# Kernel optimization log

Measured on AMD Instinct MI355X. Metric: run time of the kernel, lower is better.

## Reference

```python
import jax, jax.numpy as jnp
import numpy as np

N, E = 50000, 800000
IN, H1, H2, HEADS, EMB = 128, 32, 32, 4, 128
NEG_SLOPE = 0.2  # DGL GATConv default leaky_relu slope


def setup_inputs() -> dict:
    key = jax.random.key(0)
    ks = jax.random.split(key, 14)
    s = 0.05
    return {
        "x": jax.random.normal(ks[0], (N, IN), jnp.float32),
        "src": jax.random.randint(ks[1], (E,), 0, N, jnp.int32),
        "dst": jax.random.randint(ks[2], (E,), 0, N, jnp.int32),
        "W1": jax.random.normal(ks[3], (IN, HEADS * H1), jnp.float32) * s,
        "al1": jax.random.normal(ks[4], (HEADS, H1), jnp.float32) * s,
        "ar1": jax.random.normal(ks[5], (HEADS, H1), jnp.float32) * s,
        "b1": jnp.zeros((HEADS * H1,), jnp.float32),
        "W2": jax.random.normal(ks[6], (HEADS * H1, HEADS * H2), jnp.float32) * s,
        "al2": jax.random.normal(ks[7], (HEADS, H2), jnp.float32) * s,
        "ar2": jax.random.normal(ks[8], (HEADS, H2), jnp.float32) * s,
        "b2": jnp.zeros((HEADS * H2,), jnp.float32),
        "Wp": jax.random.normal(ks[9], (HEADS * H2, EMB), jnp.float32) * s,
        "bp": jnp.zeros((EMB,), jnp.float32),
    }


def gat_layer(x, W, al, ar, b, src, dst, heads, d_out):
    n = x.shape[0]
    feat = (x @ W).reshape(n, heads, d_out)            # [N,H,D]
    el = (feat * al).sum(-1)                           # [N,H]
    er = (feat * ar).sum(-1)                           # [N,H]
    e = jax.nn.leaky_relu(el[src] + er[dst], NEG_SLOPE)  # [E,H]
    # edge softmax over destination segments
    m = jax.ops.segment_max(e, dst, num_segments=n)    # [N,H] (-inf for empty)
    ex = jnp.exp(e - m[dst])                           # [E,H]
    z = jax.ops.segment_sum(ex, dst, num_segments=n)   # [N,H]
    alpha = ex / z[dst]                                # [E,H]
    msg = alpha[:, :, None] * feat[src]                # [E,H,D]
    out = jax.ops.segment_sum(msg, dst, num_segments=n)  # [N,H,D]
    return out + b.reshape(1, heads, d_out)


def reference(x, src, dst, W1, al1, ar1, b1, W2, al2, ar2, b2, Wp, bp):
    h = gat_layer(x, W1, al1, ar1, b1, src, dst, HEADS, H1).reshape(N, -1)
    h = gat_layer(h, W2, al2, ar2, b2, src, dst, HEADS, H2).reshape(N, -1)
    out = h @ Wp + bp
    return (h, out)
```

## Files before the change

### kernel.cpp

```cpp
#include <hip/hip_runtime.h>
#include <hip/hip_bf16.h>

#define N_NODES 50000
#define HEADS 4
#define DHEAD 32
#define F 128
#define NEG_SLOPE 0.2f
#define MAXD 64

typedef unsigned int uint;
typedef unsigned short ushort;
typedef __attribute__((ext_vector_type(8))) short bf16x8;
typedef __attribute__((ext_vector_type(4))) float f32x4;

__device__ __forceinline__ float bf2f(ushort u) {
    union { uint i; float f; } c; c.i = ((uint)u) << 16; return c.f;
}
__device__ __forceinline__ ushort f2bf(float f) {
    union { float f; uint i; } c; c.f = f;
    uint u = c.i + 0x7FFF + ((c.i >> 16) & 1);
    return (ushort)(u >> 16);
}
__device__ __forceinline__ float sel4(int h, float a, float b, float c, float d) {
    return (h & 2) ? ((h & 1) ? d : c) : ((h & 1) ? b : a);
}

__global__ void rank_hist_wtrans_kernel(
    const int* __restrict__ dst, int* __restrict__ counts, int* __restrict__ rank,
    const float* __restrict__ W1, const float* __restrict__ W2,
    const float* __restrict__ Wp,
    const float* __restrict__ al1, const float* __restrict__ ar1,
    const float* __restrict__ al2, const float* __restrict__ ar2,
    ushort* __restrict__ WT, int E, int EB) {
    if (blockIdx.x < (uint)EB) {
        int i = blockIdx.x * 256 + threadIdx.x;
        if (i < E) rank[i] = atomicAdd(&counts[dst[i]], 1);
        return;
    }
    int bid = blockIdx.x - EB;
    if (bid < 3) {
        const float* W = (bid == 0) ? W1 : (bid == 1) ? W2 : Wp;
        ushort* T = WT + (size_t)bid * 128 * 128;
        for (int i = threadIdx.x; i < 128 * 128; i += 256) {
            int r = i >> 7, c = i & 127;
            T[c * 128 + r] = f2bf(W[i]);
        }
    } else {
        const float* W   = (bid == 3) ? W1 : W2;
        const float* a_l = (bid == 3) ? al1 : al2;
        const float* a_r = (bid == 3) ? ar1 : ar2;
        ushort* T = WT + 3 * 128 * 128 + (bid - 3) * 16 * 128;
        for (int i = threadIdx.x; i < 16 * 128; i += 256) {
            int c = i >> 7, k = i & 127;
            float v = 0.f;
            if (c < 8) {
                int h = c & 3;
                const float* a  = (c < 4) ? (a_l + h * 32) : (a_r + h * 32);
                const float* wr = W + k * 128 + h * 32;
#pragma unroll
                for (int d = 0; d < 32; d++) v += wr[d] * a[d];
            }
            T[i] = f2bf(v);
        }
    }
}

__global__ __launch_bounds__(256) void scanA_kernel(const int* __restrict__ counts,
                                                    int* __restrict__ local_sc,
                                                    int* __restrict__ partials, int N) {
    int i = blockIdx.x * 256 + threadIdx.x;
    int v = (i < N) ? counts[i] : 0;
    int lane = threadIdx.x & 63;
    int w = threadIdx.x >> 6;
    int x = v;
#pragma unroll
    for (int off = 1; off < 64; off <<= 1) {
        int t = __shfl_up(x, off);
        if (lane >= off) x += t;
    }
    __shared__ int wsum[4];
    if (lane == 63) wsum[w] = x;
    __syncthreads();
    int wpre = 0;
#pragma unroll
    for (int k = 0; k < 4; k++)
        if (k < w) wpre += wsum[k];
    if (i < N) local_sc[i] = x - v + wpre;
    if (threadIdx.x == 255) partials[blockIdx.x] = wpre + x;
}

__global__ void scanB_kernel(int* __restrict__ partials, int NP) {
    int tid = threadIdx.x;
    int v = (tid < NP) ? partials[tid] : 0;
    int lane = tid & 63;
    int w = tid >> 6;
    int x = v;
#pragma unroll
    for (int off = 1; off < 64; off <<= 1) {
        int t = __shfl_up(x, off);
        if (lane >= off) x += t;
    }
    __shared__ int wsum[4];
    if (lane == 63) wsum[w] = x;
    __syncthreads();
    int wpre = 0;
#pragma unroll
    for (int k = 0; k < 4; k++)
        if (k < w) wpre += wsum[k];
    if (tid < NP) partials[tid] = x - v + wpre;
}

__global__ __launch_bounds__(256) void scanC_kernel(int* __restrict__ offs,
                                                    const int* __restrict__ partials,
                                                    int N, int E) {
    int i = blockIdx.x * 256 + threadIdx.x;
    if (i < N) offs[i] += partials[blockIdx.x];
    if (i == 0) offs[N] = E;
}

__global__ void posfix_kernel(const int* __restrict__ dst, const int* __restrict__ offs,
                              int* __restrict__ rank, int E) {
    int i = blockIdx.x * 256 + threadIdx.x;
    if (i < E) rank[i] += offs[dst[i]];
}

#define SCH 2048
__global__ __launch_bounds__(256) void scatter_ranged_kernel(
    const int* __restrict__ src, const int* __restrict__ pos,
    int* __restrict__ csr_src, int E) {
    int range = blockIdx.x & 7;
    int chunk = blockIdx.x >> 3;
    int base = chunk * SCH + threadIdx.x;
    int lo = (int)(((long long)range * E) >> 3);
    int hi = (int)(((long long)(range + 1) * E) >> 3);
#pragma unroll
    for (int k = 0; k < SCH / 256; k++) {
        int i = base + k * 256;
        if (i < E) {
            int p = pos[i];
            if (p >= lo && p < hi) csr_src[p] = src[i];
        }
    }
}

template <bool A_FP32, bool OUT_BF16, bool BIAS, bool ELER>
__global__ __launch_bounds__(256) void mfma_gemm_kernel(
    const void* __restrict__ Av, const ushort* __restrict__ BT,
    const float* __restrict__ bias, const ushort* __restrict__ ALR,
    void* __restrict__ Cv, float* __restrict__ el, float* __restrict__ er, int M) {
    int wid = threadIdx.x >> 6;
    int lane = threadIdx.x & 63;
    int row0 = blockIdx.x * 64 + wid * 16;
    int rsub = lane & 15;
    int kg = lane >> 4;
    int row = row0 + rsub;
    int rowc = (row < M) ? row : (M - 1);

    bf16x8 af[4];
    if (A_FP32) {
        const float* A = (const float*)Av;
        const float* ap = A + (size_t)rowc * 128 + kg * 8;
#pragma unroll
        for (int ks = 0; ks < 4; ks++) {
            float4 lo = *(const float4*)(ap + ks * 32);
            float4 hi = *(const float4*)(ap + ks * 32 + 4);
            bf16x8 v;
            v[0] = (short)f2bf(lo.x); v[1] = (short)f2bf(lo.y);
            v[2] = (short)f2bf(lo.z); v[3] = (short)f2bf(lo.w);
            v[4] = (short)f2bf(hi.x); v[5] = (short)f2bf(hi.y);
            v[6] = (short)f2bf(hi.z); v[7] = (short)f2bf(hi.w);
            af[ks] = v;
        }
    } else {
        const ushort* A = (const ushort*)Av;
        const ushort* ap = A + (size_t)rowc * 128 + kg * 8;
#pragma unroll
        for (int ks = 0; ks < 4; ks++) af[ks] = *(const bf16x8*)(ap + ks * 32);
    }

    f32x4 acc[8];
#pragma unroll
    for (int ct = 0; ct < 8; ct++) acc[ct] = (f32x4){0.f, 0.f, 0.f, 0.f};

    const ushort* bp = BT + (size_t)rsub * 128 + kg * 8;
#pragma unroll
    for (int ks = 0; ks < 4; ks++) {
#pragma unroll
        for (int ct = 0; ct < 8; ct++) {
            bf16x8 bf = *(const bf16x8*)(bp + (size_t)ct * 16 * 128 + ks * 32);
            acc[ct] = __builtin_amdgcn_mfma_f32_16x16x32_bf16(af[ks], bf, acc[ct], 0, 0, 0);
        }
    }

    f32x4 acce = (f32x4){0.f, 0.f, 0.f, 0.f};
    if (ELER) {
        const ushort* ep = ALR + rsub * 128 + kg * 8;
#pragma unroll
        for (int ks = 0; ks < 4; ks++) {
            bf16x8 eb = *(const bf16x8*)(ep + ks * 32);
            acce = __builtin_amdgcn_mfma_f32_16x16x32_bf16(af[ks], eb, acce, 0, 0, 0);
        }
    }

    if (row0 >= M) return;

#pragma unroll
    for (int ct = 0; ct < 8; ct++) {
        int col = ct * 16 + rsub;
        float bv = BIAS ? bias[col] : 0.f;
#pragma unroll
        for (int r = 0; r < 4; r++) {
            int gr = row0 + kg * 4 + r;
            if (gr < M) {
                float v = acc[ct][r] + bv;
                if (OUT_BF16) ((ushort*)Cv)[(size_t)gr * 128 + col] = f2bf(v);
                else          ((float*)Cv)[(size_t)gr * 128 + col] = v;
            }
        }
    }

    if (ELER && rsub < 8) {
#pragma unroll
        for (int r = 0; r < 4; r++) {
            int gr = row0 + kg * 4 + r;
            if (gr < M) {
                if (rsub < 4) el[(size_t)gr * 4 + rsub] = acce[r];
                else          er[(size_t)gr * 4 + (rsub - 4)] = acce[r];
            }
        }
    }
}

template <bool F32OUT>
__global__ __launch_bounds__(256) void aggregate_kernel(
    const ushort* __restrict__ featb, const float* __restrict__ el,
    const float* __restrict__ er, const float* __restrict__ bias,
    const int* __restrict__ offsets, const int* __restrict__ csr_src,
    void* __restrict__ outv, int N) {
    __shared__ int   s_sv[16][MAXD + 1];
    __shared__ float s_lg[16][MAXD + 1][4];
    int tid = threadIdx.x;
    int gl = tid & 15;
    int g  = tid >> 4;
    int lane = tid & 63;
    int n = blockIdx.x * 16 + g;
    if (n >= N) return;
    int start = offsets[n], end = offsets[n + 1];
    int deg = end - start;
    bool fast = (deg <= MAXD);

    float4 erv = *(const float4*)(er + (size_t)n * 4);
    float er_h[4] = {erv.x, erv.y, erv.z, erv.w};

    float m[4], s[4];
#pragma unroll
    for (int h = 0; h < 4; h++) { m[h] = -1e30f; s[h] = 0.f; }

    for (int e = start + gl; e < end; e += 16) {
        int sv = csr_src[e];
        float4 ev = *(const float4*)(el + (size_t)sv * 4);
        float elh[4] = {ev.x, ev.y, ev.z, ev.w};
        int idx = e - start;
        if (fast) s_sv[g][idx] = sv;
#pragma unroll
        for (int h = 0; h < 4; h++) {
            float v = elh[h] + er_h[h];
            v = (v >= 0.f) ? v : NEG_SLOPE * v;
            if (fast) s_lg[g][idx][h] = v;
            float mn = fmaxf(m[h], v);
            s[h] = s[h] * __expf(m[h] - mn) + __expf(v - mn);
            m[h] = mn;
        }
    }
#pragma unroll
    for (int off = 1; off < 16; off <<= 1) {
#pragma unroll
        for (int h = 0; h < 4; h++) {
            float mo = __shfl_xor(m[h], off);
            float so = __shfl_xor(s[h], off);
            float mn = fmaxf(m[h], mo);
            s[h] = s[h] * __expf(m[h] - mn) + so * __expf(mo - mn);
            m[h] = mn;
        }
    }

    int h0 = gl >> 2;
    int c0 = gl * 8;
    float acc[8] = {};

    if (fast) {
        float rz[4];
#pragma unroll
        for (int h = 0; h < 4; h++) rz[h] = (deg > 0) ? 1.0f / s[h] : 0.f;
        for (int e = gl; e < deg; e += 16) {
#pragma unroll
            for (int h = 0; h < 4; h++)
                s_lg[g][e][h] = __expf(s_lg[g][e][h] - m[h]) * rz[h];
        }
        for (int e0 = 0; e0 < deg; e0 += 8) {
            int nb = deg - e0; if (nb > 8) nb = 8;
            float av[8]; int svv[8];
#pragma unroll
            for (int jj = 0; jj < 8; jj++) {
                int idx = (jj < nb) ? (e0 + jj) : e0;
                svv[jj] = s_sv[g][idx];
                av[jj] = (jj < nb) ? s_lg[g][idx][h0] : 0.f;
            }
#pragma unroll
            for (int jj = 0; jj < 8; jj++) {
                uint4 f0 = *(const uint4*)(featb + (size_t)svv[jj] * 128 + c0);
                acc[0] = fmaf(av[jj], bf2f(f0.x & 0xFFFF), acc[0]);
                acc[1] = fmaf(av[jj], bf2f(f0.x >> 16),    acc[1]);
                acc[2] = fmaf(av[jj], bf2f(f0.y & 0xFFFF), acc[2]);
                acc[3] = fmaf(av[jj], bf2f(f0.y >> 16),    acc[3]);
                acc[4] = fmaf(av[jj], bf2f(f0.z & 0xFFFF), acc[4]);
                acc[5] = fmaf(av[jj], bf2f(f0.z >> 16),    acc[5]);
                acc[6] = fmaf(av[jj], bf2f(f0.w & 0xFFFF), acc[6]);
                acc[7] = fmaf(av[jj], bf2f(f0.w >> 16),    acc[7]);
            }
        }
    } else {
        float mh  = sel4(h0, m[0], m[1], m[2], m[3]);
        float sh  = sel4(h0, s[0], s[1], s[2], s[3]);
        float rzh = (deg > 0) ? 1.0f / sh : 0.f;
        int j = gl & 3;
        float erh = sel4(h0, er_h[0], er_h[1], er_h[2], er_h[3]);
        int bidx = lane & 60;
        for (int e = start; e < end; e += 4) {
            int rem = end - e;
            int ej = e + ((j < rem) ? j : 0);
            int svj = csr_src[ej];
            float v = el[(size_t)svj * 4 + h0] + erh;
            v = (v >= 0.f) ? v : NEG_SLOPE * v;
            float a = __expf(v - mh) * rzh;
            if (j >= rem) a = 0.f;
#pragma unroll
            for (int jj = 0; jj < 4; jj++) {
                float ajj = __shfl(a, bidx | jj);
                int svjj  = __shfl(svj, bidx | jj);
                uint4 f0 = *(const uint4*)(featb + (size_t)svjj * 128 + c0);
                acc[0] = fmaf(ajj, bf2f(f0.x & 0xFFFF), acc[0]);
                acc[1] = fmaf(ajj, bf2f(f0.x >> 16),    acc[1]);
                acc[2] = fmaf(ajj, bf2f(f0.y & 0xFFFF), acc[2]);
                acc[3] = fmaf(ajj, bf2f(f0.y >> 16),    acc[3]);
                acc[4] = fmaf(ajj, bf2f(f0.z & 0xFFFF), acc[4]);
                acc[5] = fmaf(ajj, bf2f(f0.z >> 16),    acc[5]);
                acc[6] = fmaf(ajj, bf2f(f0.w & 0xFFFF), acc[6]);
                acc[7] = fmaf(ajj, bf2f(f0.w >> 16),    acc[7]);
            }
        }
    }

    float4 b0 = *(const float4*)(bias + c0);
    float4 b1 = *(const float4*)(bias + c0 + 4);
    float o[8];
    o[0] = acc[0] + b0.x; o[1] = acc[1] + b0.y; o[2] = acc[2] + b0.z; o[3] = acc[3] + b0.w;
    o[4] = acc[4] + b1.x; o[5] = acc[5] + b1.y; o[6] = acc[6] + b1.z; o[7] = acc[7] + b1.w;
    if (F32OUT) {
        float* outf = (float*)outv;
        float4 w0, w1;
        w0.x = o[0]; w0.y = o[1]; w0.z = o[2]; w0.w = o[3];
        w1.x = o[4]; w1.y = o[5]; w1.z = o[6]; w1.w = o[7];
        *(float4*)(outf + (size_t)n * 128 + c0) = w0;
        *(float4*)(outf + (size_t)n * 128 + c0 + 4) = w1;
    } else {
        ushort* outb = (ushort*)outv;
        uint4 p;
        p.x = (uint)f2bf(o[0]) | ((uint)f2bf(o[1]) << 16);
        p.y = (uint)f2bf(o[2]) | ((uint)f2bf(o[3]) << 16);
        p.z = (uint)f2bf(o[4]) | ((uint)f2bf(o[5]) << 16);
        p.w = (uint)f2bf(o[6]) | ((uint)f2bf(o[7]) << 16);
        *(uint4*)(outb + (size_t)n * 128 + c0) = p;
    }
}

extern "C" void kernel_launch(void* const* d_in, const int* in_sizes, int n_in,
                              void* d_out, int out_size, void* d_ws, size_t ws_size,
                              hipStream_t stream) {
    const float* x   = (const float*)d_in[0];
    const int*   src = (const int*)d_in[1];
    const int*   dst = (const int*)d_in[2];
    const float* W1  = (const float*)d_in[3];
    const float* al1 = (const float*)d_in[4];
    const float* ar1 = (const float*)d_in[5];
    const float* b1  = (const float*)d_in[6];
    const float* W2  = (const float*)d_in[7];
    const float* al2 = (const float*)d_in[8];
    const float* ar2 = (const float*)d_in[9];
    const float* b2  = (const float*)d_in[10];
    const float* Wp  = (const float*)d_in[11];
    const float* bp  = (const float*)d_in[12];

    const int N = in_sizes[0] / F;
    const int E = in_sizes[1];

    float* h_out = (float*)d_out;
    float* p_out = h_out + (size_t)N * F;

    const int NB = (N + 255) / 256;
    const int EB = (E + 255) / 256;

    char* w = (char*)d_ws;
    ushort* featb   = (ushort*)w;
    ushort* h1b     = featb + (size_t)N * F;
    float* el       = (float*)(h1b + (size_t)N * F);
    float* er       = el + (size_t)N * 4;
    int*   offs     = (int*)(er + (size_t)N * 4);
    int*   counts   = offs + (N + 1);
    int*   rank     = counts + N;
    int*   csrsrc   = rank + E;
    int*   partials = csrsrc + E;
    ushort* WT      = (ushort*)(partials + 256);

    ushort* WT1  = WT;
    ushort* WT2  = WT + 128 * 128;
    ushort* WTp  = WT + 2 * 128 * 128;
    ushort* ALR1 = WT + 3 * 128 * 128;
    ushort* ALR2 = ALR1 + 16 * 128;

    hipMemsetAsync(counts, 0, (size_t)N * 4, stream);
    rank_hist_wtrans_kernel<<<EB + 5, 256, 0, stream>>>(
        dst, counts, rank, W1, W2, Wp, al1, ar1, al2, ar2, WT, E, EB);
    scanA_kernel<<<NB, 256, 0, stream>>>(counts, offs, partials, N);
    scanB_kernel<<<1, 256, 0, stream>>>(partials, NB);
    scanC_kernel<<<NB, 256, 0, stream>>>(offs, partials, N, E);
    posfix_kernel<<<EB, 256, 0, stream>>>(dst, offs, rank, E);
    scatter_ranged_kernel<<<8 * ((E + SCH - 1) / SCH), 256, 0, stream>>>(src, rank, csrsrc, E);

    int ggrid = (N + 63) / 64;
    int agrid = (N + 15) / 16;

    mfma_gemm_kernel<true, true, false, true><<<ggrid, 256, 0, stream>>>(
        x, WT1, nullptr, ALR1, featb, el, er, N);
    aggregate_kernel<false><<<agrid, 256, 0, stream>>>(
        featb, el, er, b1, offs, csrsrc, h1b, N);

    mfma_gemm_kernel<false, true, false, true><<<ggrid, 256, 0, stream>>>(
        h1b, WT2, nullptr, ALR2, featb, el, er, N);
    aggregate_kernel<true><<<agrid, 256, 0, stream>>>(
        featb, el, er, b2, offs, csrsrc, h_out, N);

    mfma_gemm_kernel<true, false, true, false><<<ggrid, 256, 0, stream>>>(
        h_out, WTp, bp, nullptr, p_out, nullptr, nullptr, N);
}
```

Baseline: 239.4 us.

## Build CSR with range-partitioned atomic cursors instead of per-edge rank arrays

Measured after the change: 256.0 us. 6.9% more time.

```diff
diff --git a/kernel.cpp b/kernel.cpp
--- a/kernel.cpp
+++ b/kernel.cpp
@@ -7,6 +7,7 @@
 #define F 128
 #define NEG_SLOPE 0.2f
 #define MAXD 64
+#define SCH 2048
 
 typedef unsigned int uint;
 typedef unsigned short ushort;
@@ -25,19 +26,30 @@
     return (h & 2) ? ((h & 1) ? d : c) : ((h & 1) ? b : a);
 }
 
-__global__ void rank_hist_wtrans_kernel(
-    const int* __restrict__ dst, int* __restrict__ counts, int* __restrict__ rank,
+__global__ void hist_ranged_wtrans_kernel(
+    const int* __restrict__ dst, int* __restrict__ counts,
     const float* __restrict__ W1, const float* __restrict__ W2,
     const float* __restrict__ Wp,
     const float* __restrict__ al1, const float* __restrict__ ar1,
     const float* __restrict__ al2, const float* __restrict__ ar2,
-    ushort* __restrict__ WT, int E, int EB) {
-    if (blockIdx.x < (uint)EB) {
-        int i = blockIdx.x * 256 + threadIdx.x;
-        if (i < E) rank[i] = atomicAdd(&counts[dst[i]], 1);
+    ushort* __restrict__ WT, int E, int N, int EC) {
+    if (blockIdx.x < (uint)(8 * EC)) {
+        int range = blockIdx.x & 7;
+        int chunk = blockIdx.x >> 3;
+        int base = chunk * SCH + threadIdx.x;
+        int nlo = (int)(((long long)range * N) >> 3);
+        int nhi = (int)(((long long)(range + 1) * N) >> 3);
+#pragma unroll
+        for (int k = 0; k < SCH / 256; k++) {
+            int i = base + k * 256;
+            if (i < E) {
+                int d = dst[i];
+                if (d >= nlo && d < nhi) atomicAdd(&counts[d], 1);
+            }
+        }
         return;
     }
-    int bid = blockIdx.x - EB;
+    int bid = blockIdx.x - 8 * EC;
     if (bid < 3) {
         const float* W = (bid == 0) ? W1 : (bid == 1) ? W2 : Wp;
         ushort* T = WT + (size_t)bid * 128 * 128;
@@ -111,34 +123,35 @@
 }
 
 __global__ __launch_bounds__(256) void scanC_kernel(int* __restrict__ offs,
+                                                    int* __restrict__ cursor,
                                                     const int* __restrict__ partials,
                                                     int N, int E) {
     int i = blockIdx.x * 256 + threadIdx.x;
-    if (i < N) offs[i] += partials[blockIdx.x];
+    if (i < N) {
+        int o = offs[i] + partials[blockIdx.x];
+        offs[i] = o;
+        cursor[i] = o;
+    }
     if (i == 0) offs[N] = E;
 }
 
-__global__ void posfix_kernel(const int* __restrict__ dst, const int* __restrict__ offs,
-                              int* __restrict__ rank, int E) {
-    int i = blockIdx.x * 256 + threadIdx.x;
-    if (i < E) rank[i] += offs[dst[i]];
-}
-
-#define SCH 2048
-__global__ __launch_bounds__(256) void scatter_ranged_kernel(
-    const int* __restrict__ src, const int* __restrict__ pos,
-    int* __restrict__ csr_src, int E) {
+__global__ __launch_bounds__(256) void scatter_fused_kernel(
+    const int* __restrict__ src, const int* __restrict__ dst,
+    int* __restrict__ cursor, int* __restrict__ csr_src, int E, int N) {
     int range = blockIdx.x & 7;
     int chunk = blockIdx.x >> 3;
     int base = chunk * SCH + threadIdx.x;
-    int lo = (int)(((long long)range * E) >> 3);
-    int hi = (int)(((long long)(range + 1) * E) >> 3);
+    int nlo = (int)(((long long)range * N) >> 3);
+    int nhi = (int)(((long long)(range + 1) * N) >> 3);
 #pragma unroll
     for (int k = 0; k < SCH / 256; k++) {
         int i = base + k * 256;
         if (i < E) {
-            int p = pos[i];
-            if (p >= lo && p < hi) csr_src[p] = src[i];
+            int d = dst[i];
+            if (d >= nlo && d < nhi) {
+                int p = atomicAdd(&cursor[d], 1);
+                csr_src[p] = src[i];
+            }
         }
     }
 }
@@ -398,7 +411,7 @@
     float* p_out = h_out + (size_t)N * F;
 
     const int NB = (N + 255) / 256;
-    const int EB = (E + 255) / 256;
+    const int EC = (E + SCH - 1) / SCH;
 
     char* w = (char*)d_ws;
     ushort* featb   = (ushort*)w;
@@ -407,8 +420,8 @@
     float* er       = el + (size_t)N * 4;
     int*   offs     = (int*)(er + (size_t)N * 4);
     int*   counts   = offs + (N + 1);
-    int*   rank     = counts + N;
-    int*   csrsrc   = rank + E;
+    int*   cursor   = counts + N;
+    int*   csrsrc   = cursor + N;
     int*   partials = csrsrc + E;
     ushort* WT      = (ushort*)(partials + 256);
 
@@ -419,13 +432,12 @@
     ushort* ALR2 = ALR1 + 16 * 128;
 
     hipMemsetAsync(counts, 0, (size_t)N * 4, stream);
-    rank_hist_wtrans_kernel<<<EB + 5, 256, 0, stream>>>(
-        dst, counts, rank, W1, W2, Wp, al1, ar1, al2, ar2, WT, E, EB);
+    hist_ranged_wtrans_kernel<<<8 * EC + 5, 256, 0, stream>>>(
+        dst, counts, W1, W2, Wp, al1, ar1, al2, ar2, WT, E, N, EC);
     scanA_kernel<<<NB, 256, 0, stream>>>(counts, offs, partials, N);
     scanB_kernel<<<1, 256, 0, stream>>>(partials, NB);
-    scanC_kernel<<<NB, 256, 0, stream>>>(offs, partials, N, E);
-    posfix_kernel<<<EB, 256, 0, stream>>>(dst, offs, rank, E);
-    scatter_ranged_kernel<<<8 * ((E + SCH - 1) / SCH), 256, 0, stream>>>(src, rank, csrsrc, E);
+    scanC_kernel<<<NB, 256, 0, stream>>>(offs, cursor, partials, N, E);
+    scatter_fused_kernel<<<8 * EC, 256, 0, stream>>>(src, dst, cursor, csrsrc, E, N);
 
     int ggrid = (N + 63) / 64;
     int agrid = (N + 15) / 16;
```

## Replace global atomic degree histogram with per-chunk LDS histograms

Applied to the files above, without the earlier changes.

Result: faster. 223.4 us (median of 2 runs) (-6.7%).

```diff
diff --git a/kernel.cpp b/kernel.cpp
--- a/kernel.cpp
+++ b/kernel.cpp
@@ -7,6 +7,9 @@
 #define F 128
 #define NEG_SLOPE 0.2f
 #define MAXD 64
+#define SCH 2048
+#define NCHUNK 64
+#define RSZ_MAX 6256
 
 typedef unsigned int uint;
 typedef unsigned short ushort;
@@ -25,19 +28,33 @@
     return (h & 2) ? ((h & 1) ? d : c) : ((h & 1) ? b : a);
 }
 
-__global__ void rank_hist_wtrans_kernel(
-    const int* __restrict__ dst, int* __restrict__ counts, int* __restrict__ rank,
+__global__ __launch_bounds__(256) void hist_lds_wtrans_kernel(
+    const int* __restrict__ dst, int* __restrict__ parthist,
+    int* __restrict__ lrank,
     const float* __restrict__ W1, const float* __restrict__ W2,
     const float* __restrict__ Wp,
     const float* __restrict__ al1, const float* __restrict__ ar1,
     const float* __restrict__ al2, const float* __restrict__ ar2,
-    ushort* __restrict__ WT, int E, int EB) {
-    if (blockIdx.x < (uint)EB) {
-        int i = blockIdx.x * 256 + threadIdx.x;
-        if (i < E) rank[i] = atomicAdd(&counts[dst[i]], 1);
+    ushort* __restrict__ WT, int E, int N, int CH, int RSZ) {
+    __shared__ int lhist[RSZ_MAX];
+    if (blockIdx.x < (uint)(8 * NCHUNK)) {
+        int r = blockIdx.x & 7;
+        int c = blockIdx.x >> 3;
+        int nlo = r * RSZ;
+        int nhi = nlo + RSZ; if (nhi > N) nhi = N;
+        for (int j = threadIdx.x; j < RSZ; j += 256) lhist[j] = 0;
+        __syncthreads();
+        int lo = c * CH, hi = lo + CH; if (hi > E) hi = E;
+        for (int i = lo + threadIdx.x; i < hi; i += 256) {
+            int d = dst[i];
+            if (d >= nlo && d < nhi) lrank[i] = atomicAdd(&lhist[d - nlo], 1);
+        }
+        __syncthreads();
+        int* ph = parthist + (size_t)(r * NCHUNK + c) * RSZ;
+        for (int j = threadIdx.x; j < RSZ; j += 256) ph[j] = lhist[j];
         return;
     }
-    int bid = blockIdx.x - EB;
+    int bid = blockIdx.x - 8 * NCHUNK;
     if (bid < 3) {
         const float* W = (bid == 0) ? W1 : (bid == 1) ? W2 : Wp;
         ushort* T = WT + (size_t)bid * 128 * 128;
@@ -65,14 +82,26 @@
     }
 }
 
-__global__ __launch_bounds__(256) void scanA_kernel(const int* __restrict__ counts,
+__global__ __launch_bounds__(256) void scanA_kernel(int* __restrict__ parthist,
                                                     int* __restrict__ local_sc,
-                                                    int* __restrict__ partials, int N) {
+                                                    int* __restrict__ partials,
+                                                    int N, int RSZ) {
     int i = blockIdx.x * 256 + threadIdx.x;
-    int v = (i < N) ? counts[i] : 0;
+    int deg = 0;
+    if (i < N) {
+        int r = i / RSZ;
+        int li = i - r * RSZ;
+        size_t base = (size_t)(r * NCHUNK) * RSZ + li;
+        for (int c = 0; c < NCHUNK; c++) {
+            size_t idx = base + (size_t)c * RSZ;
+            int t = parthist[idx];
+            parthist[idx] = deg;
+            deg += t;
+        }
+    }
     int lane = threadIdx.x & 63;
     int w = threadIdx.x >> 6;
-    int x = v;
+    int x = deg;
 #pragma unroll
     for (int off = 1; off < 64; off <<= 1) {
         int t = __shfl_up(x, off);
@@ -85,7 +114,7 @@
 #pragma unroll
     for (int k = 0; k < 4; k++)
         if (k < w) wpre += wsum[k];
-    if (i < N) local_sc[i] = x - v + wpre;
+    if (i < N) local_sc[i] = x - deg + wpre;
     if (threadIdx.x == 255) partials[blockIdx.x] = wpre + x;
 }
 
@@ -118,13 +147,20 @@
     if (i == 0) offs[N] = E;
 }
 
-__global__ void posfix_kernel(const int* __restrict__ dst, const int* __restrict__ offs,
-                              int* __restrict__ rank, int E) {
+__global__ void posfix_kernel(const int* __restrict__ dst,
+                              const int* __restrict__ offs,
+                              const int* __restrict__ parthist,
+                              int* __restrict__ lrank, int E, int CH, int RSZ) {
     int i = blockIdx.x * 256 + threadIdx.x;
-    if (i < E) rank[i] += offs[dst[i]];
-}
-
-#define SCH 2048
+    if (i < E) {
+        int d = dst[i];
+        int c = i / CH;
+        int r = d / RSZ;
+        int li = d - r * RSZ;
+        lrank[i] += offs[d] + parthist[(size_t)(r * NCHUNK + c) * RSZ + li];
+    }
+}
+
 __global__ __launch_bounds__(256) void scatter_ranged_kernel(
     const int* __restrict__ src, const int* __restrict__ pos,
     int* __restrict__ csr_src, int E) {
@@ -397,8 +433,10 @@
     float* h_out = (float*)d_out;
     float* p_out = h_out + (size_t)N * F;
 
-    const int NB = (N + 255) / 256;
-    const int EB = (E + 255) / 256;
+    const int NB  = (N + 255) / 256;
+    const int ECS = (E + SCH - 1) / SCH;
+    const int CH  = (E + NCHUNK - 1) / NCHUNK;
+    const int RSZ = (N + 7) / 8;
 
     char* w = (char*)d_ws;
     ushort* featb   = (ushort*)w;
@@ -406,11 +444,11 @@
     float* el       = (float*)(h1b + (size_t)N * F);
     float* er       = el + (size_t)N * 4;
     int*   offs     = (int*)(er + (size_t)N * 4);
-    int*   counts   = offs + (N + 1);
-    int*   rank     = counts + N;
-    int*   csrsrc   = rank + E;
+    int*   lrank    = offs + (N + 1);
+    int*   csrsrc   = lrank + E;
     int*   partials = csrsrc + E;
-    ushort* WT      = (ushort*)(partials + 256);
+    int*   parthist = partials + 256;
+    ushort* WT      = (ushort*)(parthist + (size_t)8 * NCHUNK * RSZ);
 
     ushort* WT1  = WT;
     ushort* WT2  = WT + 128 * 128;
@@ -418,14 +456,13 @@
     ushort* ALR1 = WT + 3 * 128 * 128;
     ushort* ALR2 = ALR1 + 16 * 128;
 
-    hipMemsetAsync(counts, 0, (size_t)N * 4, stream);
-    rank_hist_wtrans_kernel<<<EB + 5, 256, 0, stream>>>(
-        dst, counts, rank, W1, W2, Wp, al1, ar1, al2, ar2, WT, E, EB);
-    scanA_kernel<<<NB, 256, 0, stream>>>(counts, offs, partials, N);
+    hist_lds_wtrans_kernel<<<8 * NCHUNK + 5, 256, 0, stream>>>(
+        dst, parthist, lrank, W1, W2, Wp, al1, ar1, al2, ar2, WT, E, N, CH, RSZ);
+    scanA_kernel<<<NB, 256, 0, stream>>>(parthist, offs, partials, N, RSZ);
     scanB_kernel<<<1, 256, 0, stream>>>(partials, NB);
     scanC_kernel<<<NB, 256, 0, stream>>>(offs, partials, N, E);
-    posfix_kernel<<<EB, 256, 0, stream>>>(dst, offs, rank, E);
-    scatter_ranged_kernel<<<8 * ((E + SCH - 1) / SCH), 256, 0, stream>>>(src, rank, csrsrc, E);
+    posfix_kernel<<<(E + 255) / 256, 256, 0, stream>>>(dst, offs, parthist, lrank, E, CH, RSZ);
+    scatter_ranged_kernel<<<8 * ECS, 256, 0, stream>>>(src, lrank, csrsrc, E);
 
     int ggrid = (N + 63) / 64;
     int agrid = (N + 15) / 16;
```
